# Kernel optimization log

Hardware: AMD Instinct MI355X
Metric: run time of the kernel (lower is better)

Reference implementation:

```python
import jax, jax.numpy as jnp
import numpy as np

N = 100000   # nodes
E = 1600000  # edges (avg degree 16)
D = 64       # in_dim
H = 64       # hidden_dim
NEG_SLOPE = 0.2


def setup_inputs() -> dict:
    key = jax.random.key(0)
    ks = jax.random.split(key, 10)
    s = 0.1  # param init scale
    return {
        "x": jax.random.normal(ks[0], (N, D), jnp.float32),
        "edge_index": jax.random.randint(ks[1], (2, E), 0, N, dtype=jnp.int64),
        "h": jax.random.normal(ks[2], (1, N, H), jnp.float32),
        "c": jax.random.normal(ks[3], (1, N, H), jnp.float32),
        "W_gat": jax.random.normal(ks[4], (D, H), jnp.float32) * s,
        "att_src": jax.random.normal(ks[5], (H,), jnp.float32) * s,
        "att_dst": jax.random.normal(ks[6], (H,), jnp.float32) * s,
        "bias_gat": jax.random.normal(ks[7], (H,), jnp.float32) * s,
        "W_ih": jax.random.normal(ks[8], (4 * H, H), jnp.float32) * s,
        "W_hh": jax.random.normal(ks[9], (4 * H, H), jnp.float32) * s,
    }


def reference(x, edge_index, h, c, W_gat, att_src, att_dst, bias_gat, W_ih, W_hh):
    src, dst = edge_index[0], edge_index[1]  # message j -> i

    # ---- Breadth: GATConv (heads=1) + tanh ----
    xs = x @ W_gat                             # [N, H] projected features
    a_src = xs @ att_src                       # [N]
    a_dst = xs @ att_dst                       # [N]
    e = jax.nn.leaky_relu(a_src[src] + a_dst[dst], NEG_SLOPE)  # [E]
    # scatter-softmax over incoming edges of each destination node
    m = jax.lax.stop_gradient(jax.ops.segment_max(e, dst, num_segments=N))
    p = jnp.exp(e - m[dst])
    z = jax.ops.segment_sum(p, dst, num_segments=N)
    alpha = p / (z[dst] + 1e-16)               # [E]
    agg = jax.ops.segment_sum(xs[src] * alpha[:, None], dst, num_segments=N)
    xb = jnp.tanh(agg + bias_gat)              # [N, H]

    # ---- Depth: single-step bias-free LSTM ----
    h0, c0 = h[0], c[0]                        # [N, H]
    gates = xb @ W_ih.T + h0 @ W_hh.T          # [N, 4H]
    i, f, g, o = jnp.split(gates, 4, axis=-1)  # torch gate order i,f,g,o
    c1 = jax.nn.sigmoid(f) * c0 + jax.nn.sigmoid(i) * jnp.tanh(g)
    h1 = jax.nn.sigmoid(o) * jnp.tanh(c1)
    return h1, h1[None], c1[None]
```

## Files before the change

kernel.cpp:

```cpp
#include <hip/hip_runtime.h>
#include <cmath>

#define NN 100000
#define EE 1600000
#define NB 1563
#define CAP 1344
#define EPB 25

using bf16x8 = __attribute__((ext_vector_type(8))) __bf16;
using f32x4  = __attribute__((ext_vector_type(4))) float;

__device__ __forceinline__ unsigned short f2bf(float f) {
  __bf16 b = (__bf16)f;
  return __builtin_bit_cast(unsigned short, b);
}
__device__ __forceinline__ float bflo(unsigned int u) {
  return __uint_as_float(u << 16);
}
__device__ __forceinline__ float bfhi(unsigned int u) {
  return __uint_as_float(u & 0xffff0000u);
}
__device__ __forceinline__ float sigmoidf_(float v) {
  return 1.0f / (1.0f + __expf(-v));
}
__device__ __forceinline__ bf16x8 cvt8(float4 a, float4 b) {
  bf16x8 r;
  r[0]=(__bf16)a.x; r[1]=(__bf16)a.y; r[2]=(__bf16)a.z; r[3]=(__bf16)a.w;
  r[4]=(__bf16)b.x; r[5]=(__bf16)b.y; r[6]=(__bf16)b.z; r[7]=(__bf16)b.w;
  return r;
}

__global__ __launch_bounds__(128) void k_prep(
    const float* __restrict__ Wih, const float* __restrict__ Whh,
    const float* __restrict__ Wg,
    unsigned short* __restrict__ wperm, unsigned short* __restrict__ wgp)
{
  if (blockIdx.x < 256) {
    const int p = blockIdx.x, k = threadIdx.x;
    const int g = p & 3;
    const int h = (p >> 4) + ((p >> 2) & 3) * 16;
    const int row = g*64 + h;
    const float v = (k < 64) ? Wih[row*64 + k] : Whh[row*64 + (k - 64)];
    wperm[p*128 + k] = f2bf(v);
  } else {
    for (int idx = threadIdx.x; idx < 4096; idx += 128) {
      const int lane = idx >> 6, r = idx & 63;
      const int nt = r >> 4, kf = (r >> 3) & 1, j = r & 7;
      const int m = lane & 15, quad = lane >> 4;
      wgp[idx] = f2bf(Wg[(kf*32 + quad*8 + j)*64 + nt*16 + m]);
    }
  }
}

__global__ __launch_bounds__(256) void k_proj(
    const float* __restrict__ x, const unsigned short* __restrict__ wgp,
    const float* __restrict__ att_s, const float* __restrict__ att_d,
    unsigned short* __restrict__ xs16, float* __restrict__ a_src,
    float* __restrict__ a_dst)
{
  const int lane = threadIdx.x & 63;
  const int wave = threadIdx.x >> 6;
  const int tile = blockIdx.x * 4 + wave;
  if (tile >= NN / 16) return;
  const int m = lane & 15, quad = lane >> 4;

  bf16x8 bfrag[4][2];
  {
    const unsigned short* wp = wgp + lane*64;
    #pragma unroll
    for (int nt = 0; nt < 4; ++nt)
      #pragma unroll
      for (int kf = 0; kf < 2; ++kf)
        bfrag[nt][kf] = *(const bf16x8*)(wp + nt*16 + kf*8);
  }

  const int row = tile*16 + m;
  bf16x8 afrag[2];
  #pragma unroll
  for (int kf = 0; kf < 2; ++kf) {
    const float4* p = (const float4*)(x + (size_t)row*64 + kf*32 + quad*8);
    afrag[kf] = cvt8(p[0], p[1]);
  }

  f32x4 acc[4];
  #pragma unroll
  for (int nt = 0; nt < 4; ++nt) acc[nt] = f32x4{0.f, 0.f, 0.f, 0.f};
  #pragma unroll
  for (int nt = 0; nt < 4; ++nt)
    #pragma unroll
    for (int kf = 0; kf < 2; ++kf)
      acc[nt] = __builtin_amdgcn_mfma_f32_16x16x32_bf16(
          afrag[kf], bfrag[nt][kf], acc[nt], 0, 0, 0);

  float ss[4] = {0.f,0.f,0.f,0.f}, sd[4] = {0.f,0.f,0.f,0.f};
  #pragma unroll
  for (int nt = 0; nt < 4; ++nt) {
    const float av = att_s[nt*16 + m], dv = att_d[nt*16 + m];
    #pragma unroll
    for (int r = 0; r < 4; ++r) {
      const float v = acc[nt][r];
      xs16[(size_t)(tile*16 + quad*4 + r)*64 + nt*16 + m] = f2bf(v);
      ss[r] += v * av;
      sd[r] += v * dv;
    }
  }
  #pragma unroll
  for (int off = 1; off < 16; off <<= 1) {
    #pragma unroll
    for (int r = 0; r < 4; ++r) {
      ss[r] += __shfl_xor(ss[r], off);
      sd[r] += __shfl_xor(sd[r], off);
    }
  }
  if (m == 0) {
    #pragma unroll
    for (int r = 0; r < 4; ++r) {
      a_src[tile*16 + quad*4 + r] = ss[r];
      a_dst[tile*16 + quad*4 + r] = sd[r];
    }
  }
}

__global__ __launch_bounds__(256) void k_bin(const int* __restrict__ ei,
    int* __restrict__ bcursor, unsigned int* __restrict__ binned)
{
  __shared__ int cnt[NB];
  __shared__ int gbase[NB];
  const int tid = threadIdx.x;
  const size_t base = (size_t)blockIdx.x * 256 * EPB;

  for (int b = tid; b < NB; b += 256) cnt[b] = 0;
  __syncthreads();

  unsigned int pay[EPB];
  int bidx[EPB], pos[EPB];
  #pragma unroll
  for (int j = 0; j < EPB; ++j) {
    const size_t e = base + (size_t)j*256 + tid;
    if (e < EE) {
      const int s = ei[e];
      const int d = ei[EE + e];
      bidx[j] = d >> 6;
      pay[j] = (unsigned)s | ((unsigned)(d & 63) << 17);
      pos[j] = atomicAdd(&cnt[bidx[j]], 1);
    } else {
      bidx[j] = -1;
    }
  }
  __syncthreads();

  for (int b = tid; b < NB; b += 256) {
    const int c = cnt[b];
    gbase[b] = c ? atomicAdd(&bcursor[b*16], c) : 0;
  }
  __syncthreads();

  #pragma unroll
  for (int j = 0; j < EPB; ++j) {
    if (bidx[j] >= 0) {
      const int g = gbase[bidx[j]] + pos[j];
      if (g < CAP) binned[(size_t)bidx[j]*CAP + g] = pay[j];
    }
  }
}

__global__ __launch_bounds__(256) void k_agg(
    const int* __restrict__ bcursor, const unsigned int* __restrict__ binned,
    const float* __restrict__ a_src, const float* __restrict__ a_dst,
    const unsigned short* __restrict__ xs16, const float* __restrict__ bias,
    unsigned short* __restrict__ xb16)
{
  __shared__ unsigned int raw[CAP];
  __shared__ unsigned int csr[CAP];
  __shared__ int cnt[64], offs[64], cursor[64];
  const int b = blockIdx.x;
  const int tid = threadIdx.x;
  const int ne = min(bcursor[b*16], CAP);

  if (tid < 64) cnt[tid] = 0;
  __syncthreads();
  for (int i = tid; i < ne; i += 256) {
    const unsigned int w = binned[(size_t)b*CAP + i];
    raw[i] = w;
    atomicAdd(&cnt[(w >> 17) & 63], 1);
  }
  __syncthreads();
  if (tid < 64) {
    const int v = cnt[tid];
    int inc = v;
    #pragma unroll
    for (int dd = 1; dd < 64; dd <<= 1) {
      const int o = __shfl_up(inc, dd, 64);
      if (tid >= dd) inc += o;
    }
    offs[tid] = inc - v;
    cursor[tid] = inc - v;
  }
  __syncthreads();
  for (int i = tid; i < ne; i += 256) {
    const unsigned int w = raw[i];
    const int pos = atomicAdd(&cursor[(w >> 17) & 63], 1);
    csr[pos] = w;
  }
  __syncthreads();

  const int lane = tid & 63;
  const int wv = tid >> 6;
  const int grp = lane >> 4, l16 = lane & 15;
  const float4 b4 = *(const float4*)(bias + l16*4);
  for (int t = 0; t < 16; ++t) {
    const int nl = wv*16 + t;
    const int node = b*64 + nl;
    if (node >= NN) break;
    const int bse = offs[nl];
    const int dg = cnt[nl];
    const float ad = a_dst[node];
    float acc0=0.f, acc1=0.f, acc2=0.f, acc3=0.f, psum=0.f;
    for (int e = grp; e < dg; e += 4) {
      const int s = (int)(csr[bse + e] & 0x1FFFFu);
      float ev = a_src[s] + ad;
      ev = (ev >= 0.f) ? ev : 0.2f*ev;
      const float pv = __expf(ev);
      const uint2 rw = *(const uint2*)(xs16 + (size_t)s*64 + l16*4);
      psum += pv;
      acc0 += pv*bflo(rw.x); acc1 += pv*bfhi(rw.x);
      acc2 += pv*bflo(rw.y); acc3 += pv*bfhi(rw.y);
    }
    #pragma unroll
    for (int off = 16; off < 64; off <<= 1) {
      acc0 += __shfl_xor(acc0, off);
      acc1 += __shfl_xor(acc1, off);
      acc2 += __shfl_xor(acc2, off);
      acc3 += __shfl_xor(acc3, off);
      psum += __shfl_xor(psum, off);
    }
    if (lane < 16) {
      const float invz = 1.f/(psum + 1e-16f);
      ushort4 o;
      o.x = f2bf(tanhf(acc0*invz + b4.x));
      o.y = f2bf(tanhf(acc1*invz + b4.y));
      o.z = f2bf(tanhf(acc2*invz + b4.z));
      o.w = f2bf(tanhf(acc3*invz + b4.w));
      *(ushort4*)(xb16 + (size_t)node*64 + l16*4) = o;
    }
  }
}

__global__ __launch_bounds__(256) void k_lstm(
    const unsigned short* __restrict__ xb16, const float* __restrict__ h0,
    const float* __restrict__ c0, const unsigned short* __restrict__ wperm,
    float* __restrict__ out)
{
  const int lane = threadIdx.x & 63;
  const int wv = threadIdx.x >> 6;
  const int m = lane & 15, quad = lane >> 4;

  bf16x8 wfr[4][4];
  #pragma unroll
  for (int u = 0; u < 4; ++u) {
    const unsigned short* wr = wperm + (size_t)((wv*4 + u)*16 + m)*128;
    #pragma unroll
    for (int kf = 0; kf < 4; ++kf)
      wfr[u][kf] = *(const bf16x8*)(wr + kf*32 + quad*8);
  }

  for (int tile = blockIdx.x; tile < NN/16; tile += gridDim.x) {
    const int node = tile*16 + m;
    bf16x8 bfr[4];
    bfr[0] = *(const bf16x8*)(xb16 + (size_t)node*64 + quad*8);
    bfr[1] = *(const bf16x8*)(xb16 + (size_t)node*64 + 32 + quad*8);
    {
      const float* p0 = h0 + (size_t)node*64 + quad*8;
      bfr[2] = cvt8(*(const float4*)p0, *(const float4*)(p0 + 4));
      const float* p1 = h0 + (size_t)node*64 + 32 + quad*8;
      bfr[3] = cvt8(*(const float4*)p1, *(const float4*)(p1 + 4));
    }

    f32x4 acc[4];
    #pragma unroll
    for (int u = 0; u < 4; ++u) acc[u] = f32x4{0.f, 0.f, 0.f, 0.f};
    #pragma unroll
    for (int u = 0; u < 4; ++u)
      #pragma unroll
      for (int kf = 0; kf < 4; ++kf)
        acc[u] = __builtin_amdgcn_mfma_f32_16x16x32_bf16(
            wfr[u][kf], bfr[kf], acc[u], 0, 0, 0);

    const size_t obase = (size_t)node*64 + quad*16 + wv*4;
    const float4 cv = *(const float4*)(c0 + obase);
    const float cvv[4] = {cv.x, cv.y, cv.z, cv.w};
    float h1a[4], c1a[4];
    #pragma unroll
    for (int u = 0; u < 4; ++u) {
      const float gi = acc[u][0], gf = acc[u][1];
      const float gg = acc[u][2], go = acc[u][3];
      const float c1 = sigmoidf_(gf)*cvv[u] + sigmoidf_(gi)*tanhf(gg);
      h1a[u] = sigmoidf_(go)*tanhf(c1);
      c1a[u] = c1;
    }
    const float4 hv  = make_float4(h1a[0], h1a[1], h1a[2], h1a[3]);
    const float4 c1v = make_float4(c1a[0], c1a[1], c1a[2], c1a[3]);
    *(float4*)(out + obase) = hv;
    *(float4*)(out + (size_t)NN*64 + obase) = hv;
    *(float4*)(out + (size_t)2*NN*64 + obase) = c1v;
  }
}

extern "C" void kernel_launch(void* const* d_in, const int* in_sizes, int n_in,
                              void* d_out, int out_size, void* d_ws, size_t ws_size,
                              hipStream_t stream) {
  const float* x    = (const float*)d_in[0];
  const int*   ei   = (const int*)d_in[1];
  const float* h    = (const float*)d_in[2];
  const float* c    = (const float*)d_in[3];
  const float* Wg   = (const float*)d_in[4];
  const float* atts = (const float*)d_in[5];
  const float* attd = (const float*)d_in[6];
  const float* bg   = (const float*)d_in[7];
  const float* Wih  = (const float*)d_in[8];
  const float* Whh  = (const float*)d_in[9];
  float* out = (float*)d_out;

  char* w = (char*)d_ws;
  unsigned short* xs16  = (unsigned short*)w; w += (size_t)NN*64*2;
  unsigned short* xb16  = (unsigned short*)w; w += (size_t)NN*64*2;
  unsigned short* wperm = (unsigned short*)w; w += (size_t)256*128*2;
  unsigned short* wgp   = (unsigned short*)w; w += (size_t)4096*2;
  unsigned int*   binned= (unsigned int*)w;  w += (size_t)NB*CAP*4;
  float* a_src = (float*)w; w += (size_t)NN*4;
  float* a_dst = (float*)w; w += (size_t)NN*4;
  int* bcursor = (int*)w;   w += (size_t)NB*16*4;

  hipMemsetAsync(bcursor, 0, (size_t)NB*16*4, stream);

  k_prep <<<257, 128, 0, stream>>>(Wih, Whh, Wg, wperm, wgp);
  k_bin  <<<256, 256, 0, stream>>>(ei, bcursor, binned);
  k_proj <<<(NN/16 + 3)/4, 256, 0, stream>>>(x, wgp, atts, attd, xs16, a_src, a_dst);
  k_agg  <<<NB, 256, 0, stream>>>(bcursor, binned, a_src, a_dst, xs16, bg, xb16);
  k_lstm <<<1024, 256, 0, stream>>>(xb16, h, c, wperm, out);
}
```

Measured before the change: 301.0 us.

## Fuse binning with projection and aggregation with LSTM via LDS staging

Merges the edge-binning and feature-projection kernels into one launch split by block index, so the two independent stages can run concurrently. Fuses the LSTM step into the aggregation kernel: each block writes its 64 aggregated node rows to a swizzled LDS tile and runs the MFMA LSTM on them directly. This removes the xb16 global round trip and one launch. It also replaces tanhf with an exp-based fast tanh, which adds some error near saturation, and the fused kernel uses more LDS and registers, which may lower occupancy.

```diff
diff --git a/kernel.cpp b/kernel.cpp
--- a/kernel.cpp
+++ b/kernel.cpp
@@ -22,6 +22,9 @@
 }
 __device__ __forceinline__ float sigmoidf_(float v) {
   return 1.0f / (1.0f + __expf(-v));
+}
+__device__ __forceinline__ float tanhfast(float v) {
+  return 1.0f - 2.0f / (1.0f + __expf(2.0f * v));
 }
 __device__ __forceinline__ bf16x8 cvt8(float4 a, float4 b) {
   bf16x8 r;
@@ -52,114 +55,114 @@
   }
 }
 
-__global__ __launch_bounds__(256) void k_proj(
+__global__ __launch_bounds__(256) void k_binproj(
+    const int* __restrict__ ei, int* __restrict__ bcursor,
+    unsigned int* __restrict__ binned,
     const float* __restrict__ x, const unsigned short* __restrict__ wgp,
     const float* __restrict__ att_s, const float* __restrict__ att_d,
     unsigned short* __restrict__ xs16, float* __restrict__ a_src,
     float* __restrict__ a_dst)
 {
-  const int lane = threadIdx.x & 63;
-  const int wave = threadIdx.x >> 6;
-  const int tile = blockIdx.x * 4 + wave;
-  if (tile >= NN / 16) return;
-  const int m = lane & 15, quad = lane >> 4;
-
-  bf16x8 bfrag[4][2];
-  {
-    const unsigned short* wp = wgp + lane*64;
+  if (blockIdx.x < 256) {
+    __shared__ int cnt[NB];
+    __shared__ int gbase[NB];
+    const int tid = threadIdx.x;
+    const size_t base = (size_t)blockIdx.x * 256 * EPB;
+
+    for (int b = tid; b < NB; b += 256) cnt[b] = 0;
+    __syncthreads();
+
+    unsigned int pay[EPB];
+    int bidx[EPB], pos[EPB];
+    #pragma unroll
+    for (int j = 0; j < EPB; ++j) {
+      const size_t e = base + (size_t)j*256 + tid;
+      if (e < EE) {
+        const int s = ei[e];
+        const int d = ei[EE + e];
+        bidx[j] = d >> 6;
+        pay[j] = (unsigned)s | ((unsigned)(d & 63) << 17);
+        pos[j] = atomicAdd(&cnt[bidx[j]], 1);
+      } else {
+        bidx[j] = -1;
+      }
+    }
+    __syncthreads();
+
+    for (int b = tid; b < NB; b += 256) {
+      const int c = cnt[b];
+      gbase[b] = c ? atomicAdd(&bcursor[b*16], c) : 0;
+    }
+    __syncthreads();
+
+    #pragma unroll
+    for (int j = 0; j < EPB; ++j) {
+      if (bidx[j] >= 0) {
+        const int g = gbase[bidx[j]] + pos[j];
+        if (g < CAP) binned[(size_t)bidx[j]*CAP + g] = pay[j];
+      }
+    }
+  } else {
+    const int lane = threadIdx.x & 63;
+    const int wave = threadIdx.x >> 6;
+    const int tile = (blockIdx.x - 256) * 4 + wave;
+    if (tile >= NN / 16) return;
+    const int m = lane & 15, quad = lane >> 4;
+
+    bf16x8 bfrag[4][2];
+    {
+      const unsigned short* wp = wgp + lane*64;
+      #pragma unroll
+      for (int nt = 0; nt < 4; ++nt)
+        #pragma unroll
+        for (int kf = 0; kf < 2; ++kf)
+          bfrag[nt][kf] = *(const bf16x8*)(wp + nt*16 + kf*8);
+    }
+
+    const int row = tile*16 + m;
+    bf16x8 afrag[2];
+    #pragma unroll
+    for (int kf = 0; kf < 2; ++kf) {
+      const float4* p = (const float4*)(x + (size_t)row*64 + kf*32 + quad*8);
+      afrag[kf] = cvt8(p[0], p[1]);
+    }
+
+    f32x4 acc[4];
+    #pragma unroll
+    for (int nt = 0; nt < 4; ++nt) acc[nt] = f32x4{0.f, 0.f, 0.f, 0.f};
     #pragma unroll
     for (int nt = 0; nt < 4; ++nt)
       #pragma unroll
       for (int kf = 0; kf < 2; ++kf)
-        bfrag[nt][kf] = *(const bf16x8*)(wp + nt*16 + kf*8);
-  }
-
-  const int row = tile*16 + m;
-  bf16x8 afrag[2];
-  #pragma unroll
-  for (int kf = 0; kf < 2; ++kf) {
-    const float4* p = (const float4*)(x + (size_t)row*64 + kf*32 + quad*8);
-    afrag[kf] = cvt8(p[0], p[1]);
-  }
-
-  f32x4 acc[4];
-  #pragma unroll
-  for (int nt = 0; nt < 4; ++nt) acc[nt] = f32x4{0.f, 0.f, 0.f, 0.f};
-  #pragma unroll
-  for (int nt = 0; nt < 4; ++nt)
-    #pragma unroll
-    for (int kf = 0; kf < 2; ++kf)
-      acc[nt] = __builtin_amdgcn_mfma_f32_16x16x32_bf16(
-          afrag[kf], bfrag[nt][kf], acc[nt], 0, 0, 0);
-
-  float ss[4] = {0.f,0.f,0.f,0.f}, sd[4] = {0.f,0.f,0.f,0.f};
-  #pragma unroll
-  for (int nt = 0; nt < 4; ++nt) {
-    const float av = att_s[nt*16 + m], dv = att_d[nt*16 + m];
-    #pragma unroll
-    for (int r = 0; r < 4; ++r) {
-      const float v = acc[nt][r];
-      xs16[(size_t)(tile*16 + quad*4 + r)*64 + nt*16 + m] = f2bf(v);
-      ss[r] += v * av;
-      sd[r] += v * dv;
-    }
-  }
-  #pragma unroll
-  for (int off = 1; off < 16; off <<= 1) {
-    #pragma unroll
-    for (int r = 0; r < 4; ++r) {
-      ss[r] += __shfl_xor(ss[r], off);
-      sd[r] += __shfl_xor(sd[r], off);
-    }
-  }
-  if (m == 0) {
-    #pragma unroll
-    for (int r = 0; r < 4; ++r) {
-      a_src[tile*16 + quad*4 + r] = ss[r];
-      a_dst[tile*16 + quad*4 + r] = sd[r];
-    }
-  }
-}
-
-__global__ __launch_bounds__(256) void k_bin(const int* __restrict__ ei,
-    int* __restrict__ bcursor, unsigned int* __restrict__ binned)
-{
-  __shared__ int cnt[NB];
-  __shared__ int gbase[NB];
-  const int tid = threadIdx.x;
-  const size_t base = (size_t)blockIdx.x * 256 * EPB;
-
-  for (int b = tid; b < NB; b += 256) cnt[b] = 0;
-  __syncthreads();
-
-  unsigned int pay[EPB];
-  int bidx[EPB], pos[EPB];
-  #pragma unroll
-  for (int j = 0; j < EPB; ++j) {
-    const size_t e = base + (size_t)j*256 + tid;
-    if (e < EE) {
-      const int s = ei[e];
-      const int d = ei[EE + e];
-      bidx[j] = d >> 6;
-      pay[j] = (unsigned)s | ((unsigned)(d & 63) << 17);
-      pos[j] = atomicAdd(&cnt[bidx[j]], 1);
-    } else {
-      bidx[j] = -1;
-    }
-  }
-  __syncthreads();
-
-  for (int b = tid; b < NB; b += 256) {
-    const int c = cnt[b];
-    gbase[b] = c ? atomicAdd(&bcursor[b*16], c) : 0;
-  }
-  __syncthreads();
-
-  #pragma unroll
-  for (int j = 0; j < EPB; ++j) {
-    if (bidx[j] >= 0) {
-      const int g = gbase[bidx[j]] + pos[j];
-      if (g < CAP) binned[(size_t)bidx[j]*CAP + g] = pay[j];
+        acc[nt] = __builtin_amdgcn_mfma_f32_16x16x32_bf16(
+            afrag[kf], bfrag[nt][kf], acc[nt], 0, 0, 0);
+
+    float ss[4] = {0.f,0.f,0.f,0.f}, sd[4] = {0.f,0.f,0.f,0.f};
+    #pragma unroll
+    for (int nt = 0; nt < 4; ++nt) {
+      const float av = att_s[nt*16 + m], dv = att_d[nt*16 + m];
+      #pragma unroll
+      for (int r = 0; r < 4; ++r) {
+        const float v = acc[nt][r];
+        xs16[(size_t)(tile*16 + quad*4 + r)*64 + nt*16 + m] = f2bf(v);
+        ss[r] += v * av;
+        sd[r] += v * dv;
+      }
+    }
+    #pragma unroll
+    for (int off = 1; off < 16; off <<= 1) {
+      #pragma unroll
+      for (int r = 0; r < 4; ++r) {
+        ss[r] += __shfl_xor(ss[r], off);
+        sd[r] += __shfl_xor(sd[r], off);
+      }
+    }
+    if (m == 0) {
+      #pragma unroll
+      for (int r = 0; r < 4; ++r) {
+        a_src[tile*16 + quad*4 + r] = ss[r];
+        a_dst[tile*16 + quad*4 + r] = sd[r];
+      }
     }
   }
 }
@@ -168,11 +171,13 @@
     const int* __restrict__ bcursor, const unsigned int* __restrict__ binned,
     const float* __restrict__ a_src, const float* __restrict__ a_dst,
     const unsigned short* __restrict__ xs16, const float* __restrict__ bias,
-    unsigned short* __restrict__ xb16)
+    const unsigned short* __restrict__ wperm, const float* __restrict__ h0,
+    const float* __restrict__ c0, float* __restrict__ out)
 {
   __shared__ unsigned int raw[CAP];
   __shared__ unsigned int csr[CAP];
   __shared__ int cnt[64], offs[64], cursor[64];
+  __shared__ unsigned short xb_lds[64*64];
   const int b = blockIdx.x;
   const int tid = threadIdx.x;
   const int ne = min(bcursor[b*16], CAP);
@@ -237,24 +242,17 @@
     if (lane < 16) {
       const float invz = 1.f/(psum + 1e-16f);
       ushort4 o;
-      o.x = f2bf(tanhf(acc0*invz + b4.x));
-      o.y = f2bf(tanhf(acc1*invz + b4.y));
-      o.z = f2bf(tanhf(acc2*invz + b4.z));
-      o.w = f2bf(tanhf(acc3*invz + b4.w));
-      *(ushort4*)(xb16 + (size_t)node*64 + l16*4) = o;
-    }
-  }
-}
-
-__global__ __launch_bounds__(256) void k_lstm(
-    const unsigned short* __restrict__ xb16, const float* __restrict__ h0,
-    const float* __restrict__ c0, const unsigned short* __restrict__ wperm,
-    float* __restrict__ out)
-{
-  const int lane = threadIdx.x & 63;
-  const int wv = threadIdx.x >> 6;
-  const int m = lane & 15, quad = lane >> 4;
-
+      o.x = f2bf(tanhfast(acc0*invz + b4.x));
+      o.y = f2bf(tanhfast(acc1*invz + b4.y));
+      o.z = f2bf(tanhfast(acc2*invz + b4.z));
+      o.w = f2bf(tanhfast(acc3*invz + b4.w));
+      *(ushort4*)(xb_lds + nl*64 + (((l16*4)) ^ ((nl & 7) << 3))) = o;
+    }
+  }
+  __syncthreads();
+
+  const int m = l16;
+  const int quad = grp;
   bf16x8 wfr[4][4];
   #pragma unroll
   for (int u = 0; u < 4; ++u) {
@@ -264,11 +262,15 @@
       wfr[u][kf] = *(const bf16x8*)(wr + kf*32 + quad*8);
   }
 
-  for (int tile = blockIdx.x; tile < NN/16; tile += gridDim.x) {
-    const int node = tile*16 + m;
+  #pragma unroll
+  for (int nt = 0; nt < 4; ++nt) {
+    if (b*64 + nt*16 >= NN) break;
+    const int row = nt*16 + m;
+    const int node = b*64 + row;
+    const int sw = (row & 7) << 3;
     bf16x8 bfr[4];
-    bfr[0] = *(const bf16x8*)(xb16 + (size_t)node*64 + quad*8);
-    bfr[1] = *(const bf16x8*)(xb16 + (size_t)node*64 + 32 + quad*8);
+    bfr[0] = *(const bf16x8*)(xb_lds + row*64 + ((      quad*8) ^ sw));
+    bfr[1] = *(const bf16x8*)(xb_lds + row*64 + ((32 + quad*8) ^ sw));
     {
       const float* p0 = h0 + (size_t)node*64 + quad*8;
       bfr[2] = cvt8(*(const float4*)p0, *(const float4*)(p0 + 4));
@@ -294,8 +296,8 @@
     for (int u = 0; u < 4; ++u) {
       const float gi = acc[u][0], gf = acc[u][1];
       const float gg = acc[u][2], go = acc[u][3];
-      const float c1 = sigmoidf_(gf)*cvv[u] + sigmoidf_(gi)*tanhf(gg);
-      h1a[u] = sigmoidf_(go)*tanhf(c1);
+      const float c1 = sigmoidf_(gf)*cvv[u] + sigmoidf_(gi)*tanhfast(gg);
+      h1a[u] = sigmoidf_(go)*tanhfast(c1);
       c1a[u] = c1;
     }
     const float4 hv  = make_float4(h1a[0], h1a[1], h1a[2], h1a[3]);
@@ -323,7 +325,6 @@
 
   char* w = (char*)d_ws;
   unsigned short* xs16  = (unsigned short*)w; w += (size_t)NN*64*2;
-  unsigned short* xb16  = (unsigned short*)w; w += (size_t)NN*64*2;
   unsigned short* wperm = (unsigned short*)w; w += (size_t)256*128*2;
   unsigned short* wgp   = (unsigned short*)w; w += (size_t)4096*2;
   unsigned int*   binned= (unsigned int*)w;  w += (size_t)NB*CAP*4;
@@ -333,9 +334,9 @@
 
   hipMemsetAsync(bcursor, 0, (size_t)NB*16*4, stream);
 
-  k_prep <<<257, 128, 0, stream>>>(Wih, Whh, Wg, wperm, wgp);
-  k_bin  <<<256, 256, 0, stream>>>(ei, bcursor, binned);
-  k_proj <<<(NN/16 + 3)/4, 256, 0, stream>>>(x, wgp, atts, attd, xs16, a_src, a_dst);
-  k_agg  <<<NB, 256, 0, stream>>>(bcursor, binned, a_src, a_dst, xs16, bg, xb16);
-  k_lstm <<<1024, 256, 0, stream>>>(xb16, h, c, wperm, out);
-}
+  k_prep    <<<257, 128, 0, stream>>>(Wih, Whh, Wg, wperm, wgp);
+  k_binproj <<<256 + (NN/16 + 3)/4, 256, 0, stream>>>(
+      ei, bcursor, binned, x, wgp, atts, attd, xs16, a_src, a_dst);
+  k_agg     <<<NB, 256, 0, stream>>>(
+      bcursor, binned, a_src, a_dst, xs16, bg, wperm, h, c, out);
+}
```

Measured after the change: 320.0 us. 1.06x slower.
